# Kernel optimization log

Hardware: AMD Instinct MI355X
Metric: run time of the kernel (lower is better)

Reference implementation:

```python
import jax, jax.numpy as jnp
import numpy as np

B, S, D, H = 2, 2048, 1024, 16
HD = D // H  # head_dim = 64


def setup_inputs() -> dict:
    rng = jax.random.key(0)
    ks = jax.random.split(rng, 14)
    s = 0.02
    return {
        "query": jax.random.normal(ks[0], (B, S, D), jnp.float32),
        "key": jax.random.normal(ks[1], (B, S, D), jnp.float32),
        "value": jax.random.normal(ks[2], (B, S, D), jnp.float32),
        "Wq": jax.random.normal(ks[3], (D, D), jnp.float32) * s,
        "bq": jnp.zeros((D,), jnp.float32),
        "Wk": jax.random.normal(ks[4], (D, D), jnp.float32) * s,
        "bk": jnp.zeros((D,), jnp.float32),
        "Wv": jax.random.normal(ks[5], (D, D), jnp.float32) * s,
        "bv": jnp.zeros((D,), jnp.float32),
        "Wo": jax.random.normal(ks[6], (D, D), jnp.float32) * s,
        "bo": jnp.zeros((D,), jnp.float32),
        "Wa": jax.random.normal(ks[7], (3, D, D), jnp.float32) * s,  # 3 aspect projections
        "ba": jnp.zeros((3, D), jnp.float32),
    }


def reference(query, key, value, Wq, bq, Wk, bk, Wv, bv, Wo, bo, Wa, ba):
    scale = 1.0 / jnp.sqrt(jnp.asarray(HD, query.dtype))
    # projections; split heads -> [B, H, S, HD]
    q = (query @ Wq + bq).reshape(B, S, H, HD).transpose(0, 2, 1, 3)
    k = (key @ Wk + bk).reshape(B, S, H, HD).transpose(0, 2, 1, 3)
    v = (value @ Wv + bv).reshape(B, S, H, HD).transpose(0, 2, 1, 3)
    # main attention (dropout p=0, no masks)
    logits = jnp.einsum('bhqd,bhkd->bhqk', q, k) * scale
    attn_weights = jax.nn.softmax(logits, axis=-1)  # [B, H, S, S]
    ctx = jnp.einsum('bhqk,bhkd->bhqd', attn_weights, v)
    attn_output = ctx.transpose(0, 2, 1, 3).reshape(B, S, D) @ Wo + bo
    # 3 interpretable aspect patterns: each proj applied to query and key,
    # full-dim QK^T scaled by sqrt(head_dim), softmax over keys.
    q_asp = jnp.einsum('bsd,ade->abse', query, Wa) + ba[:, None, None, :]
    k_asp = jnp.einsum('bsd,ade->abse', key, Wa) + ba[:, None, None, :]
    pat_logits = jnp.einsum('abqd,abkd->abqk', q_asp, k_asp) * scale
    patterns = jax.nn.softmax(pat_logits, axis=-1)  # [3, B, S, S]
    return attn_output, attn_weights, patterns
```

## Files before the change

kernel.cpp:

```cpp
#include <hip/hip_runtime.h>

typedef unsigned short u16;
typedef short s16x4 __attribute__((ext_vector_type(4)));
typedef short s16x8 __attribute__((ext_vector_type(8)));
typedef float f32x4 __attribute__((ext_vector_type(4)));

#define DEVFN __device__ __forceinline__

constexpr long AW_OFF  = 4194304;
constexpr long PAT_OFF = AW_OFF + 134217728;

DEVFN u16 f2bf(float x) {
  unsigned u = __builtin_bit_cast(unsigned, x);
  unsigned r = (u + 0x7fffu + ((u >> 16) & 1u)) >> 16;
  return (u16)r;
}

DEVFN void gld16(const u16* g, u16* l) {
  __builtin_amdgcn_global_load_lds(
      (const __attribute__((address_space(1))) unsigned int*)g,
      (__attribute__((address_space(3))) unsigned int*)l, 16, 0, 0);
}

__global__ __launch_bounds__(256) void k_cvt(const float* __restrict__ in,
                                             u16* __restrict__ out, int n4) {
  int i = blockIdx.x * 256 + threadIdx.x;
  if (i >= n4) return;
  float4 v = ((const float4*)in)[i];
  s16x4 o; o[0] = f2bf(v.x); o[1] = f2bf(v.y); o[2] = f2bf(v.z); o[3] = f2bf(v.w);
  ((s16x4*)out)[i] = o;
}

template <bool IN_F32>
__global__ __launch_bounds__(256) void k_tr(const void* __restrict__ inv,
                                            u16* __restrict__ out,
                                            long ldin, long ldout,
                                            long inz1, long inz2, long outz, int zdiv) {
  __shared__ u16 tile[32][33];
  int z = blockIdx.z;
  long ioff = (long)(z / zdiv) * inz1 + (long)(z % zdiv) * inz2;
  int k0 = blockIdx.y * 32, n0 = blockIdx.x * 32;
  int tx = threadIdx.x, ty = threadIdx.y;
#pragma unroll
  for (int i = 0; i < 4; ++i) {
    long k = k0 + ty + i * 8, n = n0 + tx;
    u16 v;
    if constexpr (IN_F32) v = f2bf(((const float*)inv)[ioff + k * ldin + n]);
    else                  v = ((const u16*)inv)[ioff + k * ldin + n];
    tile[ty + i * 8][tx] = v;
  }
  __syncthreads();
  long ooff = (long)z * outz;
#pragma unroll
  for (int i = 0; i < 4; ++i) {
    long n = n0 + ty + i * 8, k = k0 + tx;
    out[ooff + n * ldout + k] = tile[tx][ty + i * 8];
  }
}

template <typename OutT, int EPI>
__global__ __launch_bounds__(256) void k_gemm_nt(
    const u16* __restrict__ Ap, const u16* __restrict__ Bp, OutT* __restrict__ Cp,
    const float* __restrict__ bias, const float* __restrict__ rinv, float alpha, int K,
    long lda, long ldb, long ldc,
    long saz1, long saz2, long sbz1, long sbz2, long scz1, long scz2,
    long sbias, int zdiv) {
  __shared__ __align__(16) u16 At[128][64];
  __shared__ __align__(16) u16 Bt[128][64];
  const int tid = threadIdx.x, lane = tid & 63, wid = tid >> 6;
  const int wm = wid >> 1, wn = wid & 1;
  const int z = blockIdx.z, z1 = z / zdiv, z2 = z % zdiv;
  const u16* Ab = Ap + (long)z1 * saz1 + (long)z2 * saz2;
  const u16* Bb = Bp + (long)z1 * sbz1 + (long)z2 * sbz2;
  OutT* C = Cp + (long)z1 * scz1 + (long)z2 * scz2;
  const float* bz = bias ? bias + (long)z * sbias : nullptr;
  const int row0 = blockIdx.y * 128, col0 = blockIdx.x * 128;
  const int lk = lane & 15, g = lane >> 4;

  f32x4 acc[4][4] = {};

  for (int k0 = 0; k0 < K; k0 += 64) {
#pragma unroll
    for (int it = 0; it < 4; ++it) {
      const int u = it * 256 + tid;
      const int r = u >> 3, p = u & 7;
      const int cg = (p ^ (r & 7)) * 8;
      gld16(Ab + (long)(row0 + r) * lda + (k0 + cg), &At[r][p * 8]);
      gld16(Bb + (long)(col0 + r) * ldb + (k0 + cg), &Bt[r][p * 8]);
    }
    __syncthreads();
#pragma unroll
    for (int kk = 0; kk < 2; ++kk) {
      s16x8 af[4], bf[4];
#pragma unroll
      for (int m = 0; m < 4; ++m)
        af[m] = *(const s16x8*)&At[wm * 64 + m * 16 + lk][((kk * 4 + g) ^ (lk & 7)) * 8];
#pragma unroll
      for (int n = 0; n < 4; ++n)
        bf[n] = *(const s16x8*)&Bt[wn * 64 + n * 16 + lk][((kk * 4 + g) ^ (lk & 7)) * 8];
#pragma unroll
      for (int m = 0; m < 4; ++m)
#pragma unroll
        for (int n = 0; n < 4; ++n)
          acc[m][n] = __builtin_amdgcn_mfma_f32_16x16x32_bf16(af[m], bf[n], acc[m][n], 0, 0, 0);
    }
    __syncthreads();
  }

  const float* rz = (EPI == 1) ? rinv + (long)z * 2048 : nullptr;
#pragma unroll
  for (int m = 0; m < 4; ++m) {
    const int grow = row0 + wm * 64 + m * 16 + g * 4;
#pragma unroll
    for (int r = 0; r < 4; ++r) {
      float iv = 0.0f;
      if constexpr (EPI == 1) iv = rz[grow + r];
#pragma unroll
      for (int n = 0; n < 4; ++n) {
        const int gcol = col0 + wn * 64 + n * 16 + lk;
        float v;
        if constexpr (EPI == 1) v = __expf(alpha * acc[m][n][r]) * iv;
        else                    v = alpha * acc[m][n][r] + (bz ? bz[gcol] : 0.0f);
        if constexpr (sizeof(OutT) == 2) C[(long)(grow + r) * ldc + gcol] = f2bf(v);
        else                             C[(long)(grow + r) * ldc + gcol] = v;
      }
    }
  }
}

__global__ __launch_bounds__(256) void k_flash(
    const u16* __restrict__ qp, const u16* __restrict__ kp, const u16* __restrict__ vt,
    u16* __restrict__ ctx, float* __restrict__ rinv) {
  __shared__ __align__(16) char lds[49152];
  u16* Qt = (u16*)lds;
  u16* Kt = (u16*)(lds + 16384);
  u16* Vl = (u16*)(lds + 32768);
  const int tid = threadIdx.x, lane = tid & 63, wid = tid >> 6;
  const int wk = wid >> 1, wq = wid & 1;
  const int bh = blockIdx.y, q0 = blockIdx.x * 128;
  const long qkbase = (long)(bh >> 4) * 2097152 + (long)(bh & 15) * 64;
  const long vbase = (long)bh * 131072;
  const int lk = lane & 15, g = lane >> 4;
  const int sp = lane & 7;
  const int sr = lane >> 3;

#pragma unroll
  for (int i = 0; i < 4; ++i) {
    const int rr = (wid * 4 + i) * 8 + sr;
    gld16(qp + qkbase + (long)(q0 + rr) * 1024 + ((sp ^ (rr & 7)) * 8), Qt + rr * 64 + sp * 8);
  }
  __syncthreads();

  s16x8 qf[2][4];
#pragma unroll
  for (int kk = 0; kk < 2; ++kk) {
#pragma unroll
    for (int nq = 0; nq < 4; ++nq)
      qf[kk][nq] = *(const s16x8*)(Qt + (wq * 64 + nq * 16 + lk) * 64 + ((kk * 4 + g) ^ (lk & 7)) * 8);
  }

  f32x4 cacc[4][4] = {};
  float rs[4] = {0.f, 0.f, 0.f, 0.f};

  for (int t = 0; t < 16; ++t) {
    const int kb = t * 128;
#pragma unroll
    for (int i = 0; i < 4; ++i) {
      const int rr = (wid * 4 + i) * 8 + sr;
      gld16(kp + qkbase + (long)(kb + rr) * 1024 + ((sp ^ (rr & 7)) * 8), Kt + rr * 64 + sp * 8);
      const int dd = (wid * 4 + i) * 4 + g;
      const int pv = lane & 15;
      const int cv = (pv & 8) | ((pv ^ dd) & 7);
      gld16(vt + vbase + (long)dd * 2048 + (kb + cv * 8), Vl + dd * 128 + pv * 8);
    }
    __syncthreads();

    f32x4 st[4][4] = {};
#pragma unroll
    for (int kk = 0; kk < 2; ++kk) {
      s16x8 af[4];
#pragma unroll
      for (int mk = 0; mk < 4; ++mk)
        af[mk] = *(const s16x8*)(Kt + (wk * 64 + mk * 16 + lk) * 64 + ((kk * 4 + g) ^ (lk & 7)) * 8);
#pragma unroll
      for (int mk = 0; mk < 4; ++mk)
#pragma unroll
        for (int nq = 0; nq < 4; ++nq)
          st[mk][nq] = __builtin_amdgcn_mfma_f32_16x16x32_bf16(af[mk], qf[kk][nq], st[mk][nq], 0, 0, 0);
    }
#pragma unroll
    for (int mk = 0; mk < 4; ++mk)
#pragma unroll
      for (int nq = 0; nq < 4; ++nq)
#pragma unroll
        for (int j = 0; j < 4; ++j) {
          const float p = __expf(st[mk][nq][j] * 0.125f);
          st[mk][nq][j] = p;
          rs[nq] += p;
        }
#pragma unroll
    for (int ks = 0; ks < 2; ++ks) {
      s16x8 pb[4];
#pragma unroll
      for (int nq = 0; nq < 4; ++nq) {
        s16x8 b;
#pragma unroll
        for (int j = 0; j < 4; ++j) {
          b[j]     = (short)f2bf(st[2 * ks][nq][j]);
          b[4 + j] = (short)f2bf(st[2 * ks + 1][nq][j]);
        }
        pb[nq] = b;
      }
#pragma unroll
      for (int md = 0; md < 4; ++md) {
        const int rowv = md * 16 + lk;
        const int u0 = ks * 4 + (g >> 1);
        const int p0 = wk * 8 + ((u0 ^ (rowv & 7)) & 7);
        const int p2 = wk * 8 + (((u0 + 2) ^ (rowv & 7)) & 7);
        const u16* vb0 = Vl + rowv * 128 + p0 * 8 + (g & 1) * 4;
        const u16* vb2 = Vl + rowv * 128 + p2 * 8 + (g & 1) * 4;
        s16x4 lo = *(const s16x4*)vb0;
        s16x4 hi = *(const s16x4*)vb2;
        s16x8 vf;
        vf[0] = lo[0]; vf[1] = lo[1]; vf[2] = lo[2]; vf[3] = lo[3];
        vf[4] = hi[0]; vf[5] = hi[1]; vf[6] = hi[2]; vf[7] = hi[3];
#pragma unroll
        for (int nq = 0; nq < 4; ++nq)
          cacc[md][nq] = __builtin_amdgcn_mfma_f32_16x16x32_bf16(vf, pb[nq], cacc[md][nq], 0, 0, 0);
      }
    }
    __syncthreads();
  }

#pragma unroll
  for (int nq = 0; nq < 4; ++nq) {
    rs[nq] += __shfl_xor(rs[nq], 16, 64);
    rs[nq] += __shfl_xor(rs[nq], 32, 64);
  }
  float* ctxl = (float*)lds;
  float* rsl  = (float*)(lds + 33024);
  if (wk == 1) {
#pragma unroll
    for (int md = 0; md < 4; ++md)
#pragma unroll
      for (int nq = 0; nq < 4; ++nq)
#pragma unroll
        for (int r = 0; r < 4; ++r)
          ctxl[(md * 16 + g * 4 + r) * 129 + wq * 64 + nq * 16 + lk] = cacc[md][nq][r];
    if (lane < 16)
#pragma unroll
      for (int nq = 0; nq < 4; ++nq) rsl[wq * 64 + nq * 16 + lane] = rs[nq];
  }
  __syncthreads();
  if (wk == 0) {
#pragma unroll
    for (int md = 0; md < 4; ++md)
#pragma unroll
      for (int nq = 0; nq < 4; ++nq)
#pragma unroll
        for (int r = 0; r < 4; ++r) {
          const int idx = (md * 16 + g * 4 + r) * 129 + wq * 64 + nq * 16 + lk;
          ctxl[idx] += cacc[md][nq][r];
        }
    if (lane < 16)
#pragma unroll
      for (int nq = 0; nq < 4; ++nq) {
        const int qi = wq * 64 + nq * 16 + lane;
        const float inv = 1.0f / (rsl[qi] + rs[nq]);
        rsl[qi] = inv;
        rinv[(long)bh * 2048 + q0 + qi] = inv;
      }
  }
  __syncthreads();
  const int qr = tid >> 1, half = tid & 1;
  const float inv = rsl[qr];
  u16* dst = ctx + (long)(bh >> 4) * 2097152 + (long)(q0 + qr) * 1024 + (long)(bh & 15) * 64 + half * 32;
#pragma unroll
  for (int c = 0; c < 4; ++c) {
    s16x8 o;
#pragma unroll
    for (int j = 0; j < 8; ++j) {
      const int d = half * 32 + c * 8 + j;
      o[j] = (short)f2bf(ctxl[d * 129 + qr] * inv);
    }
    ((s16x8*)dst)[c] = o;
  }
}

__global__ __launch_bounds__(256) void k_softmax(float* __restrict__ base) {
  float* p = base + (long)blockIdx.x * 2048;
  const int t = threadIdx.x;
  float4 v0 = ((const float4*)p)[t];
  float4 v1 = ((const float4*)p)[t + 256];
  float m = fmaxf(fmaxf(fmaxf(v0.x, v0.y), fmaxf(v0.z, v0.w)),
                  fmaxf(fmaxf(v1.x, v1.y), fmaxf(v1.z, v1.w)));
#pragma unroll
  for (int i = 32; i >= 1; i >>= 1) m = fmaxf(m, __shfl_xor(m, i, 64));
  __shared__ float sm[4], ss[4];
  if ((t & 63) == 0) sm[t >> 6] = m;
  __syncthreads();
  m = fmaxf(fmaxf(sm[0], sm[1]), fmaxf(sm[2], sm[3]));
  float4 e0, e1;
  e0.x = __expf(v0.x - m); e0.y = __expf(v0.y - m); e0.z = __expf(v0.z - m); e0.w = __expf(v0.w - m);
  e1.x = __expf(v1.x - m); e1.y = __expf(v1.y - m); e1.z = __expf(v1.z - m); e1.w = __expf(v1.w - m);
  float s = (e0.x + e0.y + e0.z + e0.w) + (e1.x + e1.y + e1.z + e1.w);
#pragma unroll
  for (int i = 32; i >= 1; i >>= 1) s += __shfl_xor(s, i, 64);
  if ((t & 63) == 0) ss[t >> 6] = s;
  __syncthreads();
  s = ss[0] + ss[1] + ss[2] + ss[3];
  float inv = 1.0f / s;
  e0.x *= inv; e0.y *= inv; e0.z *= inv; e0.w *= inv;
  e1.x *= inv; e1.y *= inv; e1.z *= inv; e1.w *= inv;
  ((float4*)p)[t] = e0;
  ((float4*)p)[t + 256] = e1;
}

extern "C" void kernel_launch(void* const* d_in, const int* in_sizes, int n_in,
                              void* d_out, int out_size, void* d_ws, size_t ws_size,
                              hipStream_t stream) {
  const float* query = (const float*)d_in[0];
  const float* key   = (const float*)d_in[1];
  const float* value = (const float*)d_in[2];
  const float* Wq = (const float*)d_in[3];
  const float* bq = (const float*)d_in[4];
  const float* Wk = (const float*)d_in[5];
  const float* bk = (const float*)d_in[6];
  const float* Wv = (const float*)d_in[7];
  const float* bv = (const float*)d_in[8];
  const float* Wo = (const float*)d_in[9];
  const float* bo = (const float*)d_in[10];
  const float* Wa = (const float*)d_in[11];
  const float* ba = (const float*)d_in[12];
  float* out = (float*)d_out;
  char* ws = (char*)d_ws;

  u16* qb  = (u16*)(ws + 0);
  u16* kb  = (u16*)(ws + 8388608);
  u16* vb  = (u16*)(ws + 16777216);
  u16* Wqt = (u16*)(ws + 25165824);
  u16* Wkt = (u16*)(ws + 27262976);
  u16* Wvt = (u16*)(ws + 29360128);
  u16* Wot = (u16*)(ws + 31457280);
  u16* Wat = (u16*)(ws + 33554432);
  u16* qp  = (u16*)(ws + 39845888);
  u16* kp  = (u16*)(ws + 48234496);
  u16* vp  = (u16*)(ws + 56623104);
  u16* vt  = (u16*)(ws + 65011712);
  u16* ctx = (u16*)(ws + 73400320);
  u16* qa  = (u16*)(ws + 81788928);
  u16* ka  = (u16*)(ws + 106954752);
  float* rinv = (float*)(ws + 25165824);

  dim3 b256(256);
  dim3 trb(32, 8);

  k_cvt<<<4096, b256, 0, stream>>>(query, qb, 1048576);
  k_cvt<<<4096, b256, 0, stream>>>(key,   kb, 1048576);
  k_cvt<<<4096, b256, 0, stream>>>(value, vb, 1048576);

  k_tr<true><<<dim3(32, 32, 1), trb, 0, stream>>>(Wq, Wqt, 1024, 1024, 0, 0, 0, 1);
  k_tr<true><<<dim3(32, 32, 1), trb, 0, stream>>>(Wk, Wkt, 1024, 1024, 0, 0, 0, 1);
  k_tr<true><<<dim3(32, 32, 1), trb, 0, stream>>>(Wv, Wvt, 1024, 1024, 0, 0, 0, 1);
  k_tr<true><<<dim3(32, 32, 1), trb, 0, stream>>>(Wo, Wot, 1024, 1024, 0, 0, 0, 1);
  k_tr<true><<<dim3(32, 32, 3), trb, 0, stream>>>(Wa, Wat, 1024, 1024, 0, 1048576, 1048576, 3);

  k_gemm_nt<u16, 0><<<dim3(8, 32, 1), b256, 0, stream>>>(
      qb, Wqt, qp, bq, nullptr, 1.0f, 1024, 1024, 1024, 1024, 0, 0, 0, 0, 0, 0, 0, 1);
  k_gemm_nt<u16, 0><<<dim3(8, 32, 1), b256, 0, stream>>>(
      kb, Wkt, kp, bk, nullptr, 1.0f, 1024, 1024, 1024, 1024, 0, 0, 0, 0, 0, 0, 0, 1);
  k_gemm_nt<u16, 0><<<dim3(8, 32, 1), b256, 0, stream>>>(
      vb, Wvt, vp, bv, nullptr, 1.0f, 1024, 1024, 1024, 1024, 0, 0, 0, 0, 0, 0, 0, 1);

  k_gemm_nt<u16, 0><<<dim3(8, 32, 3), b256, 0, stream>>>(
      qb, Wat, qa, ba, nullptr, 1.0f, 1024, 1024, 1024, 1024,
      0, 0, 0, 1048576, 0, 4194304, 1024, 3);
  k_gemm_nt<u16, 0><<<dim3(8, 32, 3), b256, 0, stream>>>(
      kb, Wat, ka, ba, nullptr, 1.0f, 1024, 1024, 1024, 1024,
      0, 0, 0, 1048576, 0, 4194304, 1024, 3);

  k_tr<false><<<dim3(2, 64, 32), trb, 0, stream>>>(
      vp, vt, 1024, 2048, 2097152, 64, 131072, 16);

  k_flash<<<dim3(16, 32), b256, 0, stream>>>(qp, kp, vt, ctx, rinv);

  k_gemm_nt<float, 1><<<dim3(16, 16, 32), b256, 0, stream>>>(
      qp, kp, out + AW_OFF, nullptr, rinv, 0.125f, 64, 1024, 1024, 2048,
      2097152, 64, 2097152, 64, 67108864, 4194304, 0, 16);

  k_gemm_nt<float, 0><<<dim3(16, 16, 6), b256, 0, stream>>>(
      qa, ka, out + PAT_OFF, nullptr, nullptr, 0.125f, 1024, 1024, 1024, 2048,
      0, 2097152, 0, 2097152, 0, 4194304, 0, 6);

  k_softmax<<<12288, b256, 0, stream>>>(out + PAT_OFF);

  k_gemm_nt<float, 0><<<dim3(8, 32, 1), b256, 0, stream>>>(
      ctx, Wot, out, bo, nullptr, 1.0f, 1024, 1024, 1024, 1024, 0, 0, 0, 0, 0, 0, 0, 1);
}
```

Measured before the change: 564.3 us.

## Batch QKV and aspect projections into fewer launches; remap blocks for XCD locality

Merges the three input conversions into one launch and packs the q/k/v biases. This lets the Q, K and V projections run as a single batched GEMM, and the query and key aspect projections as another. The GEMM and flash kernels also remap linear block IDs so consecutive tiles spread across the 8 XCDs, aiming for better L2 reuse. Fewer launches and larger grids reduce launch overhead and tail effects, at the cost of extra index arithmetic and one tiny bias-packing kernel.

```diff
diff --git a/kernel.cpp b/kernel.cpp
--- a/kernel.cpp
+++ b/kernel.cpp
@@ -22,13 +22,25 @@
       (__attribute__((address_space(3))) unsigned int*)l, 16, 0, 0);
 }
 
-__global__ __launch_bounds__(256) void k_cvt(const float* __restrict__ in,
-                                             u16* __restrict__ out, int n4) {
+__global__ __launch_bounds__(256) void k_cvt3(const float* __restrict__ a,
+                                              const float* __restrict__ b,
+                                              const float* __restrict__ c,
+                                              u16* __restrict__ out, int n4) {
   int i = blockIdx.x * 256 + threadIdx.x;
   if (i >= n4) return;
+  const float* in = (blockIdx.y == 0) ? a : (blockIdx.y == 1) ? b : c;
   float4 v = ((const float4*)in)[i];
   s16x4 o; o[0] = f2bf(v.x); o[1] = f2bf(v.y); o[2] = f2bf(v.z); o[3] = f2bf(v.w);
-  ((s16x4*)out)[i] = o;
+  ((s16x4*)(out + (long)blockIdx.y * 4194304))[i] = o;
+}
+
+__global__ __launch_bounds__(256) void k_pack3(const float* __restrict__ a,
+                                               const float* __restrict__ b,
+                                               const float* __restrict__ c,
+                                               float* __restrict__ out) {
+  int i = blockIdx.x * 256 + threadIdx.x;
+  const float* in = (i < 1024) ? a : (i < 2048) ? b : c;
+  out[i] = in[i & 1023];
 }
 
 template <bool IN_F32>
@@ -69,12 +81,19 @@
   __shared__ __align__(16) u16 Bt[128][64];
   const int tid = threadIdx.x, lane = tid & 63, wid = tid >> 6;
   const int wm = wid >> 1, wn = wid & 1;
-  const int z = blockIdx.z, z1 = z / zdiv, z2 = z % zdiv;
+
+  const int gx = gridDim.x, gy = gridDim.y;
+  int id = (blockIdx.z * gy + blockIdx.y) * gx + blockIdx.x;
+  const int nb = gx * gy * (int)gridDim.z;
+  if ((nb & 7) == 0) id = (id & 7) * (nb >> 3) + (id >> 3);
+  const int bxi = id % gx, byi = (id / gx) % gy, bzi = id / (gx * gy);
+
+  const int z = bzi, z1 = z / zdiv, z2 = z % zdiv;
   const u16* Ab = Ap + (long)z1 * saz1 + (long)z2 * saz2;
   const u16* Bb = Bp + (long)z1 * sbz1 + (long)z2 * sbz2;
   OutT* C = Cp + (long)z1 * scz1 + (long)z2 * scz2;
-  const float* bz = bias ? bias + (long)z * sbias : nullptr;
-  const int row0 = blockIdx.y * 128, col0 = blockIdx.x * 128;
+  const float* bv = bias ? bias + (long)z2 * sbias : nullptr;
+  const int row0 = byi * 128, col0 = bxi * 128;
   const int lk = lane & 15, g = lane >> 4;
 
   f32x4 acc[4][4] = {};
@@ -120,7 +139,7 @@
         const int gcol = col0 + wn * 64 + n * 16 + lk;
         float v;
         if constexpr (EPI == 1) v = __expf(alpha * acc[m][n][r]) * iv;
-        else                    v = alpha * acc[m][n][r] + (bz ? bz[gcol] : 0.0f);
+        else                    v = alpha * acc[m][n][r] + (bv ? bv[gcol] : 0.0f);
         if constexpr (sizeof(OutT) == 2) C[(long)(grow + r) * ldc + gcol] = f2bf(v);
         else                             C[(long)(grow + r) * ldc + gcol] = v;
       }
@@ -137,7 +156,13 @@
   u16* Vl = (u16*)(lds + 32768);
   const int tid = threadIdx.x, lane = tid & 63, wid = tid >> 6;
   const int wk = wid >> 1, wq = wid & 1;
-  const int bh = blockIdx.y, q0 = blockIdx.x * 128;
+
+  const int gx = gridDim.x;
+  int id = blockIdx.y * gx + blockIdx.x;
+  const int nb = gx * (int)gridDim.y;
+  if ((nb & 7) == 0) id = (id & 7) * (nb >> 3) + (id >> 3);
+  const int bh = id / gx, q0 = (id % gx) * 128;
+
   const long qkbase = (long)(bh >> 4) * 2097152 + (long)(bh & 15) * 64;
   const long vbase = (long)bh * 131072;
   const int lk = lane & 15, g = lane >> 4;
@@ -336,11 +361,7 @@
   char* ws = (char*)d_ws;
 
   u16* qb  = (u16*)(ws + 0);
-  u16* kb  = (u16*)(ws + 8388608);
-  u16* vb  = (u16*)(ws + 16777216);
   u16* Wqt = (u16*)(ws + 25165824);
-  u16* Wkt = (u16*)(ws + 27262976);
-  u16* Wvt = (u16*)(ws + 29360128);
   u16* Wot = (u16*)(ws + 31457280);
   u16* Wat = (u16*)(ws + 33554432);
   u16* qp  = (u16*)(ws + 39845888);
@@ -349,35 +370,28 @@
   u16* vt  = (u16*)(ws + 65011712);
   u16* ctx = (u16*)(ws + 73400320);
   u16* qa  = (u16*)(ws + 81788928);
-  u16* ka  = (u16*)(ws + 106954752);
-  float* rinv = (float*)(ws + 25165824);
+  float* rinv  = (float*)(ws + 25165824);
+  float* pbias = (float*)(ws + 132120576);
 
   dim3 b256(256);
   dim3 trb(32, 8);
 
-  k_cvt<<<4096, b256, 0, stream>>>(query, qb, 1048576);
-  k_cvt<<<4096, b256, 0, stream>>>(key,   kb, 1048576);
-  k_cvt<<<4096, b256, 0, stream>>>(value, vb, 1048576);
+  k_cvt3<<<dim3(4096, 3), b256, 0, stream>>>(query, key, value, qb, 1048576);
+  k_pack3<<<12, b256, 0, stream>>>(bq, bk, bv, pbias);
 
   k_tr<true><<<dim3(32, 32, 1), trb, 0, stream>>>(Wq, Wqt, 1024, 1024, 0, 0, 0, 1);
-  k_tr<true><<<dim3(32, 32, 1), trb, 0, stream>>>(Wk, Wkt, 1024, 1024, 0, 0, 0, 1);
-  k_tr<true><<<dim3(32, 32, 1), trb, 0, stream>>>(Wv, Wvt, 1024, 1024, 0, 0, 0, 1);
+  k_tr<true><<<dim3(32, 32, 1), trb, 0, stream>>>(Wk, Wqt + 1048576, 1024, 1024, 0, 0, 0, 1);
+  k_tr<true><<<dim3(32, 32, 1), trb, 0, stream>>>(Wv, Wqt + 2097152, 1024, 1024, 0, 0, 0, 1);
   k_tr<true><<<dim3(32, 32, 1), trb, 0, stream>>>(Wo, Wot, 1024, 1024, 0, 0, 0, 1);
   k_tr<true><<<dim3(32, 32, 3), trb, 0, stream>>>(Wa, Wat, 1024, 1024, 0, 1048576, 1048576, 3);
 
-  k_gemm_nt<u16, 0><<<dim3(8, 32, 1), b256, 0, stream>>>(
-      qb, Wqt, qp, bq, nullptr, 1.0f, 1024, 1024, 1024, 1024, 0, 0, 0, 0, 0, 0, 0, 1);
-  k_gemm_nt<u16, 0><<<dim3(8, 32, 1), b256, 0, stream>>>(
-      kb, Wkt, kp, bk, nullptr, 1.0f, 1024, 1024, 1024, 1024, 0, 0, 0, 0, 0, 0, 0, 1);
-  k_gemm_nt<u16, 0><<<dim3(8, 32, 1), b256, 0, stream>>>(
-      vb, Wvt, vp, bv, nullptr, 1.0f, 1024, 1024, 1024, 1024, 0, 0, 0, 0, 0, 0, 0, 1);
-
   k_gemm_nt<u16, 0><<<dim3(8, 32, 3), b256, 0, stream>>>(
+      qb, Wqt, qp, pbias, nullptr, 1.0f, 1024, 1024, 1024, 1024,
+      0, 4194304, 0, 1048576, 0, 4194304, 1024, 3);
+
+  k_gemm_nt<u16, 0><<<dim3(8, 32, 6), b256, 0, stream>>>(
       qb, Wat, qa, ba, nullptr, 1.0f, 1024, 1024, 1024, 1024,
-      0, 0, 0, 1048576, 0, 4194304, 1024, 3);
-  k_gemm_nt<u16, 0><<<dim3(8, 32, 3), b256, 0, stream>>>(
-      kb, Wat, ka, ba, nullptr, 1.0f, 1024, 1024, 1024, 1024,
-      0, 0, 0, 1048576, 0, 4194304, 1024, 3);
+      4194304, 0, 0, 1048576, 12582912, 4194304, 1024, 3);
 
   k_tr<false><<<dim3(2, 64, 32), trb, 0, stream>>>(
       vp, vt, 1024, 2048, 2097152, 64, 131072, 16);
@@ -389,7 +403,7 @@
       2097152, 64, 2097152, 64, 67108864, 4194304, 0, 16);
 
   k_gemm_nt<float, 0><<<dim3(16, 16, 6), b256, 0, stream>>>(
-      qa, ka, out + PAT_OFF, nullptr, nullptr, 0.125f, 1024, 1024, 1024, 2048,
+      qa, qa + 12582912, out + PAT_OFF, nullptr, nullptr, 0.125f, 1024, 1024, 1024, 2048,
       0, 2097152, 0, 2097152, 0, 4194304, 0, 6);
 
   k_softmax<<<12288, b256, 0, stream>>>(out + PAT_OFF);
```

New measurement: 509.5 us. -9.7%, faster.
